# Performance work log

Hardware: AMD Instinct MI355X
Metric: run time of the kernel (lower is better)

Reference implementation:

```python
import jax, jax.numpy as jnp
import numpy as np

B, TXT, IMG, D, H = 1, 512, 2048, 1024, 16
HD = D // H
MLP = 4 * D
L = TXT + IMG

def _ln(x, s, b, eps=1e-6):
    mu = jnp.mean(x, -1, keepdims=True)
    var = jnp.var(x, -1, keepdims=True)
    return (x - mu) * jax.lax.rsqrt(var + eps) * s + b

def _rms(x, scale, eps=1e-6):
    return x * jax.lax.rsqrt(jnp.mean(x * x, -1, keepdims=True) + eps) * scale

def _rope(x, pe):
    # x: [B,H,L,HD] -> pairs [B,H,L,HD/2,1,2]; pe: [1,1,L,HD/2,2,2]
    xr = x.reshape(x.shape[0], x.shape[1], x.shape[2], -1, 1, 2)
    out = pe[..., 0] * xr[..., 0] + pe[..., 1] * xr[..., 1]
    return out.reshape(x.shape)

def _mod(vec, w, b):
    m = jax.nn.silu(vec) @ w + b  # [B, 6D]
    return jnp.split(m[:, None, :], 6, axis=-1)

def _stream_qkv(x, shift, scale, n1s, n1b, qkv_w, qkv_b, qs, ks):
    xm = (1 + scale) * _ln(x, n1s, n1b) + shift
    qkv = xm @ qkv_w + qkv_b  # [B,L,3D]
    b_, l_ = qkv.shape[0], qkv.shape[1]
    qkv = qkv.reshape(b_, l_, 3, H, HD).transpose(2, 0, 3, 1, 4)  # 'B L (K H D) -> K B H L D'
    q, k, v = qkv[0], qkv[1], qkv[2]
    return _rms(q, qs), _rms(k, ks), v

def _fwd(img, txt, vec, pe,
         img_mod_w, img_mod_b, img_norm1_s, img_norm1_b, img_qkv_w, img_qkv_b,
         img_qscale, img_kscale, img_proj_w, img_proj_b, img_norm2_s, img_norm2_b,
         img_mlp_w1, img_mlp_b1, img_mlp_w2, img_mlp_b2,
         txt_mod_w, txt_mod_b, txt_norm1_s, txt_norm1_b, txt_qkv_w, txt_qkv_b,
         txt_qscale, txt_kscale, txt_proj_w, txt_proj_b, txt_norm2_s, txt_norm2_b,
         txt_mlp_w1, txt_mlp_b1, txt_mlp_w2, txt_mlp_b2):
    i_sh1, i_sc1, i_g1, i_sh2, i_sc2, i_g2 = _mod(vec, img_mod_w, img_mod_b)
    t_sh1, t_sc1, t_g1, t_sh2, t_sc2, t_g2 = _mod(vec, txt_mod_w, txt_mod_b)
    iq, ik, iv = _stream_qkv(img, i_sh1, i_sc1, img_norm1_s, img_norm1_b, img_qkv_w, img_qkv_b, img_qscale, img_kscale)
    tq, tk, tv = _stream_qkv(txt, t_sh1, t_sc1, txt_norm1_s, txt_norm1_b, txt_qkv_w, txt_qkv_b, txt_qscale, txt_kscale)
    q = jnp.concatenate((tq, iq), axis=2)  # txt tokens first
    k = jnp.concatenate((tk, ik), axis=2)
    v = jnp.concatenate((tv, iv), axis=2)
    q = _rope(q, pe)
    k = _rope(k, pe)
    logits = jnp.einsum('bhqd,bhkd->bhqk', q, k) * (HD ** -0.5)
    attn = jnp.einsum('bhqk,bhkd->bhqd', jax.nn.softmax(logits, axis=-1), v)
    attn = attn.transpose(0, 2, 1, 3).reshape(q.shape[0], L, D)  # 'B H L D -> B L (H D)'
    t_attn, i_attn = attn[:, :TXT], attn[:, TXT:]
    img = img + i_g1 * (i_attn @ img_proj_w + img_proj_b)
    h = (1 + i_sc2) * _ln(img, img_norm2_s, img_norm2_b) + i_sh2
    img = img + i_g2 * (jax.nn.gelu(h @ img_mlp_w1 + img_mlp_b1) @ img_mlp_w2 + img_mlp_b2)
    txt = txt + t_g1 * (t_attn @ txt_proj_w + txt_proj_b)
    h = (1 + t_sc2) * _ln(txt, txt_norm2_s, txt_norm2_b) + t_sh2
    txt = txt + t_g2 * (jax.nn.gelu(h @ txt_mlp_w1 + txt_mlp_b1) @ txt_mlp_w2 + txt_mlp_b2)
    return img, txt

def setup_inputs():
    key = jax.random.key(0)
    keys = iter(jax.random.split(key, 80))
    def rn(shape, s=0.02):
        return jax.random.normal(next(keys), shape, jnp.float32) * s
    inp = {
        'img': jax.random.normal(next(keys), (B, IMG, D), jnp.float32),
        'txt': jax.random.normal(next(keys), (B, TXT, D), jnp.float32),
        'vec': jax.random.normal(next(keys), (B, D), jnp.float32),
        'pe': jax.random.normal(next(keys), (1, 1, L, HD // 2, 2, 2), jnp.float32),
    }
    for p in ('img', 'txt'):
        inp[p + '_mod_w'] = rn((D, 6 * D)); inp[p + '_mod_b'] = jnp.zeros((6 * D,), jnp.float32)
        inp[p + '_norm1_s'] = jnp.ones((D,), jnp.float32); inp[p + '_norm1_b'] = jnp.zeros((D,), jnp.float32)
        inp[p + '_qkv_w'] = rn((D, 3 * D)); inp[p + '_qkv_b'] = jnp.zeros((3 * D,), jnp.float32)
        inp[p + '_qscale'] = jnp.ones((HD,), jnp.float32); inp[p + '_kscale'] = jnp.ones((HD,), jnp.float32)
        inp[p + '_proj_w'] = rn((D, D)); inp[p + '_proj_b'] = jnp.zeros((D,), jnp.float32)
        inp[p + '_norm2_s'] = jnp.ones((D,), jnp.float32); inp[p + '_norm2_b'] = jnp.zeros((D,), jnp.float32)
        inp[p + '_mlp_w1'] = rn((D, MLP)); inp[p + '_mlp_b1'] = jnp.zeros((MLP,), jnp.float32)
        inp[p + '_mlp_w2'] = rn((MLP, D)); inp[p + '_mlp_b2'] = jnp.zeros((D,), jnp.float32)
    return inp

def reference(img, txt, vec, pe,
              img_mod_w, img_mod_b, img_norm1_s, img_norm1_b, img_qkv_w, img_qkv_b,
              img_qscale, img_kscale, img_proj_w, img_proj_b, img_norm2_s, img_norm2_b,
              img_mlp_w1, img_mlp_b1, img_mlp_w2, img_mlp_b2,
              txt_mod_w, txt_mod_b, txt_norm1_s, txt_norm1_b, txt_qkv_w, txt_qkv_b,
              txt_qscale, txt_kscale, txt_proj_w, txt_proj_b, txt_norm2_s, txt_norm2_b,
              txt_mlp_w1, txt_mlp_b1, txt_mlp_w2, txt_mlp_b2):
    return _fwd(img, txt, vec, pe,
                img_mod_w, img_mod_b, img_norm1_s, img_norm1_b, img_qkv_w, img_qkv_b,
                img_qscale, img_kscale, img_proj_w, img_proj_b, img_norm2_s, img_norm2_b,
                img_mlp_w1, img_mlp_b1, img_mlp_w2, img_mlp_b2,
                txt_mod_w, txt_mod_b, txt_norm1_s, txt_norm1_b, txt_qkv_w, txt_qkv_b,
                txt_qscale, txt_kscale, txt_proj_w, txt_proj_b, txt_norm2_s, txt_norm2_b,
                txt_mlp_w1, txt_mlp_b1, txt_mlp_w2, txt_mlp_b2)
```

## Files before the change

### kernel.cpp

```cpp
#include <hip/hip_runtime.h>
#include <cstdint>
#include <cstddef>

#define DD 1024
#define HD 64
#define NH 16
#define LTXT 512
#define LIMG 2048
#define LTOT 2560
#define DMLP 4096

typedef unsigned short u16;
typedef __attribute__((ext_vector_type(8))) __bf16 bf16x8;
typedef __attribute__((ext_vector_type(4))) float f32x4;

__device__ __forceinline__ u16 f2bf(float f) {
  union { float f; uint32_t u; } v; v.f = f;
  uint32_t r = v.u + 0x7FFFu + ((v.u >> 16) & 1u);
  return (u16)(r >> 16);
}
__device__ __forceinline__ float bf2f(u16 u) {
  union { uint32_t u; float f; } v; v.u = ((uint32_t)u) << 16;
  return v.f;
}
__device__ __forceinline__ uint32_t cvtpk(float lo, float hi) {
  uint32_t r;
  asm("v_cvt_pk_bf16_f32 %0, %1, %2" : "=v"(r) : "v"(lo), "v"(hi));
  return r;
}
__device__ __forceinline__ float geluf(float x) {
  const float u = fmaf(x * x, 0.044715f, 1.0f);
  const float e = __expf(x * u * -1.5957691216057308f);
  return x / (1.f + e);
}
__device__ __forceinline__ void gload16(const void* g, void* l) {
  __builtin_amdgcn_global_load_lds(
      (const __attribute__((address_space(1))) void*)g,
      (__attribute__((address_space(3))) void*)l, 16, 0, 0);
}
#define SWZ(row) (((((row) & 3) | ((((row) >> 3) & 1) << 2)) << 4))

__global__ __launch_bounds__(256) void wcast_all(
    const float* __restrict__ s0, const float* __restrict__ s1,
    const float* __restrict__ s2, const float* __restrict__ s3,
    const float* __restrict__ s4, const float* __restrict__ s5,
    const float* __restrict__ s6, const float* __restrict__ s7,
    u16* __restrict__ d0, u16* __restrict__ d1, u16* __restrict__ d2,
    u16* __restrict__ d3, u16* __restrict__ d4, u16* __restrict__ d5,
    u16* __restrict__ d6, u16* __restrict__ d7) {
  const int b = blockIdx.x;
  const float* W; u16* Wt; int K, N, lb;
  if (b < 768)       { W = s0; Wt = d0; K = 1024; N = 3072; lb = b; }
  else if (b < 1536) { W = s1; Wt = d1; K = 1024; N = 3072; lb = b - 768; }
  else if (b < 1792) { W = s2; Wt = d2; K = 1024; N = 1024; lb = b - 1536; }
  else if (b < 2048) { W = s3; Wt = d3; K = 1024; N = 1024; lb = b - 1792; }
  else if (b < 3072) { W = s4; Wt = d4; K = 1024; N = 4096; lb = b - 2048; }
  else if (b < 4096) { W = s5; Wt = d5; K = 1024; N = 4096; lb = b - 3072; }
  else if (b < 5120) { W = s6; Wt = d6; K = 4096; N = 1024; lb = b - 4096; }
  else               { W = s7; Wt = d7; K = 4096; N = 1024; lb = b - 5120; }
  const int ntn = N >> 6;
  const int n0 = (lb % ntn) * 64, k0 = (lb / ntn) * 64;
  __shared__ float T[64][65];
  const int tx = threadIdx.x & 15, ty = threadIdx.x >> 4;
#pragma unroll
  for (int i = 0; i < 4; ++i) {
    const int r = ty + i * 16;
    const float4 v = *(const float4*)&W[(size_t)(k0 + r) * N + n0 + tx * 4];
    T[r][tx * 4 + 0] = v.x;
    T[r][tx * 4 + 1] = v.y;
    T[r][tx * 4 + 2] = v.z;
    T[r][tx * 4 + 3] = v.w;
  }
  __syncthreads();
  const int rn = threadIdx.x >> 2;
  const int cs = (threadIdx.x & 3) * 16;
  u16 buf[16];
#pragma unroll
  for (int j = 0; j < 16; ++j) buf[j] = f2bf(T[cs + j][rn]);
  u16* dst = &Wt[(size_t)(n0 + rn) * K + k0 + cs];
  *(uint4*)dst = *(uint4*)&buf[0];
  *(uint4*)(dst + 8) = *(uint4*)&buf[8];
}

__global__ __launch_bounds__(256) void mod_gemv_part(
    const float* __restrict__ vec, const float* __restrict__ wi,
    const float* __restrict__ wt, float* __restrict__ part) {
  __shared__ float sv[128];
  const int s = blockIdx.y, kc = blockIdx.z;
  const float* W = s ? wt : wi;
  if (threadIdx.x < 128) {
    float x = vec[kc * 128 + threadIdx.x];
    sv[threadIdx.x] = x / (1.f + __expf(-x));
  }
  __syncthreads();
  const int j = blockIdx.x * 256 + threadIdx.x;
  float acc = 0.f;
#pragma unroll 4
  for (int i = 0; i < 128; ++i)
    acc += sv[i] * W[(size_t)(kc * 128 + i) * 6144 + j];
  part[((size_t)(kc * 2 + s)) * 6144 + j] = acc;
}
__global__ __launch_bounds__(256) void mod_reduce(
    const float* __restrict__ part, const float* __restrict__ bi,
    const float* __restrict__ bt, float* __restrict__ modout) {
  const int idx = blockIdx.x * 256 + threadIdx.x;
  const int s = idx / 6144, j = idx % 6144;
  float a = s ? bt[j] : bi[j];
#pragma unroll
  for (int kc = 0; kc < 8; ++kc) a += part[((size_t)(kc * 2 + s)) * 6144 + j];
  modout[(size_t)s * 6144 + j] = a;
}

__global__ __launch_bounds__(256) void ln_mod2(
    const float* __restrict__ Xtxt, const float* __restrict__ Ximg,
    u16* __restrict__ out, const float* __restrict__ tns,
    const float* __restrict__ tnb, const float* __restrict__ ins,
    const float* __restrict__ inb, const float* __restrict__ modv) {
  __shared__ float red[8];
  const int r = blockIdx.x, tid = threadIdx.x;
  const float* x; const float* ns; const float* nb; const float* mv;
  if (r < LTXT) { x = Xtxt + (size_t)r * DD; ns = tns; nb = tnb; mv = modv + 6144; }
  else { x = Ximg + (size_t)(r - LTXT) * DD; ns = ins; nb = inb; mv = modv; }
  const int c0 = tid * 4;
  const float4 xv = *(const float4*)&x[c0];
  float v[4] = {xv.x, xv.y, xv.z, xv.w};
  float s = 0.f, sq = 0.f;
#pragma unroll
  for (int i = 0; i < 4; ++i) { s += v[i]; sq += v[i] * v[i]; }
#pragma unroll
  for (int o = 32; o; o >>= 1) {
    s += __shfl_xor(s, o);
    sq += __shfl_xor(sq, o);
  }
  if ((tid & 63) == 0) {
    red[tid >> 6] = s;
    red[4 + (tid >> 6)] = sq;
  }
  __syncthreads();
  s = red[0] + red[1] + red[2] + red[3];
  sq = red[4] + red[5] + red[6] + red[7];
  const float mu = s * (1.f / DD);
  const float var = sq * (1.f / DD) - mu * mu;
  const float rstd = rsqrtf(var + 1e-6f);
  const float4 nsv = *(const float4*)&ns[c0];
  const float4 nbv = *(const float4*)&nb[c0];
  const float4 shv = *(const float4*)&mv[c0];
  const float4 scv = *(const float4*)&mv[1024 + c0];
  const float nsa[4] = {nsv.x, nsv.y, nsv.z, nsv.w};
  const float nba[4] = {nbv.x, nbv.y, nbv.z, nbv.w};
  const float sha[4] = {shv.x, shv.y, shv.z, shv.w};
  const float sca[4] = {scv.x, scv.y, scv.z, scv.w};
  ushort4 o4;
  u16 ob[4];
#pragma unroll
  for (int i = 0; i < 4; ++i) {
    const float ln = (v[i] - mu) * rstd * nsa[i] + nba[i];
    ob[i] = f2bf((1.f + sca[i]) * ln + sha[i]);
  }
  o4.x = ob[0]; o4.y = ob[1]; o4.z = ob[2]; o4.w = ob[3];
  *(ushort4*)&out[(size_t)r * DD + c0] = o4;
}

__global__ __launch_bounds__(256) void resid_ln2(
    const float* __restrict__ Xtxt, const float* __restrict__ Ximg,
    const u16* __restrict__ t, const float* __restrict__ modv,
    const float* __restrict__ tns, const float* __restrict__ tnb,
    const float* __restrict__ ins, const float* __restrict__ inb,
    float* __restrict__ otxt, float* __restrict__ oimg,
    u16* __restrict__ hout) {
  __shared__ float red[8];
  const int r = blockIdx.x, tid = threadIdx.x;
  const float* x; const float* ns; const float* nb; const float* mv; float* y;
  if (r < LTXT) {
    x = Xtxt + (size_t)r * DD; ns = tns; nb = tnb; mv = modv + 6144;
    y = otxt + (size_t)r * DD;
  } else {
    x = Ximg + (size_t)(r - LTXT) * DD; ns = ins; nb = inb; mv = modv;
    y = oimg + (size_t)(r - LTXT) * DD;
  }
  const int c0 = tid * 4;
  const float4 xv = *(const float4*)&x[c0];
  const ushort4 tb = *(const ushort4*)&t[(size_t)r * DD + c0];
  const float4 gv = *(const float4*)&mv[2048 + c0];
  float v[4];
  v[0] = xv.x + gv.x * bf2f(tb.x);
  v[1] = xv.y + gv.y * bf2f(tb.y);
  v[2] = xv.z + gv.z * bf2f(tb.z);
  v[3] = xv.w + gv.w * bf2f(tb.w);
  *(float4*)&y[c0] = *(float4*)v;
  float s = 0.f, sq = 0.f;
#pragma unroll
  for (int i = 0; i < 4; ++i) { s += v[i]; sq += v[i] * v[i]; }
#pragma unroll
  for (int o = 32; o; o >>= 1) {
    s += __shfl_xor(s, o);
    sq += __shfl_xor(sq, o);
  }
  if ((tid & 63) == 0) {
    red[tid >> 6] = s;
    red[4 + (tid >> 6)] = sq;
  }
  __syncthreads();
  s = red[0] + red[1] + red[2] + red[3];
  sq = red[4] + red[5] + red[6] + red[7];
  const float mu = s * (1.f / DD);
  const float var = sq * (1.f / DD) - mu * mu;
  const float rstd = rsqrtf(var + 1e-6f);
  const float4 nsv = *(const float4*)&ns[c0];
  const float4 nbv = *(const float4*)&nb[c0];
  const float4 shv = *(const float4*)&mv[3072 + c0];
  const float4 scv = *(const float4*)&mv[4096 + c0];
  const float nsa[4] = {nsv.x, nsv.y, nsv.z, nsv.w};
  const float nba[4] = {nbv.x, nbv.y, nbv.z, nbv.w};
  const float sha[4] = {shv.x, shv.y, shv.z, shv.w};
  const float sca[4] = {scv.x, scv.y, scv.z, scv.w};
  ushort4 o4;
  u16 ob[4];
#pragma unroll
  for (int i = 0; i < 4; ++i) {
    const float ln = (v[i] - mu) * rstd * nsa[i] + nba[i];
    ob[i] = f2bf((1.f + sca[i]) * ln + sha[i]);
  }
  o4.x = ob[0]; o4.y = ob[1]; o4.z = ob[2]; o4.w = ob[3];
  *(ushort4*)&hout[(size_t)r * DD + c0] = o4;
}

__global__ __launch_bounds__(512) void gemm_pipe(
    const u16* __restrict__ A, const u16* __restrict__ BtT,
    const u16* __restrict__ BtI, const float* __restrict__ biasT,
    const float* __restrict__ biasI, u16* __restrict__ C,
    float* __restrict__ Cpart, int K, int Kblk, int N, int gelu) {
  __shared__ __align__(16) u16 As[2][128 * 32];
  __shared__ __align__(16) u16 Bs[2][128 * 32];
  const int tid = threadIdx.x, lane = tid & 63, wave = tid >> 6;
  const int nwg = gridDim.x * gridDim.y;
  const int orig = blockIdx.x + blockIdx.y * gridDim.x;
  const int lb = (orig & 7) * (nwg >> 3) + (orig >> 3);
  const int bn = lb / 20, bm = lb % 20;
  const int kc = blockIdx.z;
  const u16* Bt = (bm < (LTXT / 128)) ? BtT : BtI;
  const int wm = wave >> 1, wn = wave & 1;
  const int lr = lane & 15, lk = lane >> 4;
  f32x4 acc[2][4] = {};
  const size_t a0 = (size_t)bm * 128;
  const size_t b0 = (size_t)bn * 128;
  const int kbase = kc * Kblk;
  const int NT = Kblk >> 5;
  const int srow = tid >> 2, soff = (tid & 3) * 8;

#define STAGE(t, buf)                                                         \
  {                                                                           \
    const int k0_ = kbase + (t) * 32;                                         \
    gload16(&A[(a0 + srow) * K + k0_ + soff], &As[buf][srow * 32 + soff]);    \
    gload16(&Bt[(b0 + srow) * K + k0_ + soff], &Bs[buf][srow * 32 + soff]);   \
  }

  STAGE(0, 0);
  STAGE(1, 1);
  for (int t = 0; t < NT; ++t) {
    if (t + 1 < NT) {
      asm volatile("s_waitcnt vmcnt(2)" ::: "memory");
    } else {
      asm volatile("s_waitcnt vmcnt(0)" ::: "memory");
    }
    __builtin_amdgcn_s_barrier();
    const int b = t & 1;
    bf16x8 af[2], bfv[4];
#pragma unroll
    for (int m = 0; m < 2; ++m)
      af[m] = *(const bf16x8*)&As[b][(wm * 32 + m * 16 + lr) * 32 + lk * 8];
#pragma unroll
    for (int n = 0; n < 4; ++n)
      bfv[n] = *(const bf16x8*)&Bs[b][(wn * 64 + n * 16 + lr) * 32 + lk * 8];
    asm volatile("s_waitcnt lgkmcnt(0)" ::: "memory");
    __builtin_amdgcn_sched_barrier(0);
    __builtin_amdgcn_s_barrier();
    if (t + 2 < NT) STAGE(t + 2, b);
    __builtin_amdgcn_sched_barrier(0);
    __builtin_amdgcn_s_setprio(1);
#pragma unroll
    for (int m = 0; m < 2; ++m)
#pragma unroll
      for (int n = 0; n < 4; ++n)
        acc[m][n] = __builtin_amdgcn_mfma_f32_16x16x32_bf16(af[m], bfv[n],
                                                            acc[m][n], 0, 0, 0);
    __builtin_amdgcn_s_setprio(0);
  }
#undef STAGE

  if (Cpart) {
    float* dst = Cpart + (size_t)kc * ((size_t)LTOT * N);
#pragma unroll
    for (int n = 0; n < 4; ++n) {
      const int col = bn * 128 + wn * 64 + n * 16 + lr;
#pragma unroll
      for (int m = 0; m < 2; ++m)
#pragma unroll
        for (int r = 0; r < 4; ++r) {
          const size_t row = a0 + wm * 32 + m * 16 + lk * 4 + r;
          dst[row * (size_t)N + col] = acc[m][n][r];
        }
    }
  } else {
    const float* bias = (bm < (LTXT / 128)) ? biasT : biasI;
#pragma unroll
    for (int n = 0; n < 4; ++n) {
      const int col = bn * 128 + wn * 64 + n * 16 + lr;
      const float bv = bias[col];
#pragma unroll
      for (int m = 0; m < 2; ++m)
#pragma unroll
        for (int r = 0; r < 4; ++r) {
          const size_t row = a0 + wm * 32 + m * 16 + lk * 4 + r;
          float v = acc[m][n][r] + bv;
          if (gelu) v = geluf(v);
          C[row * (size_t)N + col] = f2bf(v);
        }
    }
  }
}

__global__ __launch_bounds__(256) void gemm_reduce(
    const float* __restrict__ part, const float* __restrict__ bT,
    const float* __restrict__ bI, u16* __restrict__ C, int N, int kcnt) {
  const size_t idx = (size_t)(blockIdx.x * 256 + threadIdx.x) * 4;
  const int row = (int)(idx / N), col = (int)(idx % N);
  float4 a = *(const float4*)&part[idx];
  for (int kc = 1; kc < kcnt; ++kc) {
    const float4 b = *(const float4*)&part[(size_t)kc * LTOT * N + idx];
    a.x += b.x; a.y += b.y; a.z += b.z; a.w += b.w;
  }
  const float* bias = (row < LTXT) ? bT : bI;
  ushort4 o;
  o.x = f2bf(a.x + bias[col]);
  o.y = f2bf(a.y + bias[col + 1]);
  o.z = f2bf(a.z + bias[col + 2]);
  o.w = f2bf(a.w + bias[col + 3]);
  *(ushort4*)&C[idx] = o;
}

__global__ __launch_bounds__(256) void gemm_reduce_gate(
    const float* __restrict__ part, const float* __restrict__ bT,
    const float* __restrict__ bI, const float* __restrict__ modv,
    float* __restrict__ otxt, float* __restrict__ oimg, int kcnt) {
  const size_t idx = (size_t)(blockIdx.x * 256 + threadIdx.x) * 4;
  const int row = (int)(idx >> 10), col = (int)(idx & 1023);
  float4 a = *(const float4*)&part[idx];
  for (int kc = 1; kc < kcnt; ++kc) {
    const float4 b = *(const float4*)&part[(size_t)kc * LTOT * DD + idx];
    a.x += b.x; a.y += b.y; a.z += b.z; a.w += b.w;
  }
  const float* bias; const float* mv; float* o;
  if (row < LTXT) {
    bias = bT; mv = modv + 6144; o = otxt + (size_t)row * DD + col;
  } else {
    bias = bI; mv = modv; o = oimg + (size_t)(row - LTXT) * DD + col;
  }
  const float4 g = *(const float4*)&mv[5120 + col];
  const float4 cur = *(const float4*)o;
  float4 r;
  r.x = cur.x + g.x * (a.x + bias[col]);
  r.y = cur.y + g.y * (a.y + bias[col + 1]);
  r.z = cur.z + g.z * (a.z + bias[col + 2]);
  r.w = cur.w + g.w * (a.w + bias[col + 3]);
  *(float4*)o = r;
}

__global__ __launch_bounds__(256) void scat_rope(
    const u16* __restrict__ qkv, u16* __restrict__ q, u16* __restrict__ k,
    const float* __restrict__ pe, const float* __restrict__ iqs,
    const float* __restrict__ iks, const float* __restrict__ tqs,
    const float* __restrict__ tks) {
  const int gw = (blockIdx.x * 256 + threadIdx.x) >> 6;
  const int lane = threadIdx.x & 63;
  const int l = gw % LTOT, h = gw / LTOT;
  const size_t rb = (size_t)l * 3072 + h * 64 + lane;
  const float qv = bf2f(qkv[rb]);
  const float kv = bf2f(qkv[rb + 1024]);
  const float* qs = (l < LTXT) ? tqs : iqs;
  const float* ks = (l < LTXT) ? tks : iks;
  const float* peb = pe + (size_t)l * 128 + (lane >> 1) * 4 + (lane & 1) * 2;
  const size_t base = ((size_t)h * LTOT + l) * HD + lane;
  {
    float ss = qv * qv;
#pragma unroll
    for (int o = 32; o; o >>= 1) ss += __shfl_xor(ss, o);
    float xn = qv * rsqrtf(ss * (1.f / HD) + 1e-6f) * qs[lane];
    float part = __shfl_xor(xn, 1);
    float x0 = (lane & 1) ? part : xn;
    float x1 = (lane & 1) ? xn : part;
    q[base] = f2bf(peb[0] * x0 + peb[1] * x1);
  }
  {
    float ss = kv * kv;
#pragma unroll
    for (int o = 32; o; o >>= 1) ss += __shfl_xor(ss, o);
    float xn = kv * rsqrtf(ss * (1.f / HD) + 1e-6f) * ks[lane];
    float part = __shfl_xor(xn, 1);
    float x0 = (lane & 1) ? part : xn;
    float x1 = (lane & 1) ? xn : part;
    k[base] = f2bf(peb[0] * x0 + peb[1] * x1);
  }
}

__global__ __launch_bounds__(256) void vt_build(const u16* __restrict__ qkv,
                                                u16* __restrict__ vt) {
  __shared__ u16 T[64][72];
  const int b = blockIdx.x;
  const int h = b & 15, lt = b >> 4;
  const int tid = threadIdx.x;
  const int r = tid >> 3, c8 = (tid & 7) * 8;
  const size_t srcbase = (size_t)(lt * 64) * 3072 + 2048 + h * 64;
  *(uint4*)&T[r][c8] = *(const uint4*)&qkv[srcbase + (size_t)r * 3072 + c8];
  *(uint4*)&T[r + 32][c8] =
      *(const uint4*)&qkv[srcbase + (size_t)(r + 32) * 3072 + c8];
  __syncthreads();
  const int d = tid >> 2, lc = (tid & 3) * 16;
  u16 buf[16];
#pragma unroll
  for (int j = 0; j < 16; ++j) buf[j] = T[lc + j][d];
  u16* dst = &vt[((size_t)h * 64 + d) * LTOT + lt * 64 + lc];
  *(uint4*)dst = *(uint4*)&buf[0];
  *(uint4*)(dst + 8) = *(uint4*)&buf[8];
}

template <int SPLIT>
__global__ __launch_bounds__(512) void attn_mfma(
    const u16* __restrict__ Q, const u16* __restrict__ Kg,
    const u16* __restrict__ VT, u16* __restrict__ out,
    float* __restrict__ part) {
  constexpr int LOG = (SPLIT == 4) ? 2 : ((SPLIT == 2) ? 1 : 0);
  __shared__ __align__(16) u16 Ks[2][64 * 64];
  __shared__ __align__(16) u16 Vs[2][64 * 64];
  const int tid = threadIdx.x, lane = tid & 63, w = tid >> 6;
  const int lr = lane & 15, lk = lane >> 4;
  const int blk = blockIdx.x;
  const int h = ((blk & 7) << 1) | ((blk >> 3) & 1);
  const int half = (blk >> 4) & (SPLIT - 1);
  const int q0 = (blk >> (4 + LOG)) * 128;
  const size_t hb = (size_t)h * LTOT;
  char* KsB0 = (char*)&Ks[0][0];
  char* VsB0 = (char*)&Vs[0][0];

  const int q = q0 + w * 16 + lr;
  const bf16x8 qa0 = *(const bf16x8*)&Q[(hb + q) * HD + lk * 8];
  const bf16x8 qa1 = *(const bf16x8*)&Q[(hb + q) * HD + 32 + lk * 8];

  const int srow = tid >> 3;
  const int soff = tid & 7;
  const int NT = (LTOT / SPLIT) / 64;
  const int kstart = half * (LTOT / SPLIT);

  float m_run = -1e30f, l_run = 0.f;
  f32x4 acc[4] = {};
  uint4 kst, vst;

  kst = *(const uint4*)&Kg[(hb + kstart + srow) * HD + soff * 8];
  vst = *(const uint4*)&VT[((size_t)h * HD + srow) * LTOT + kstart + soff * 8];
  *(uint4*)(KsB0 + ((srow * 128 + soff * 16) ^ SWZ(srow))) = kst;
  *(uint4*)(VsB0 + ((srow * 128 + soff * 16) ^ SWZ(srow))) = vst;
  __syncthreads();

  const float scale = 0.125f;
  for (int t = 0; t < NT; ++t) {
    char* KsC = KsB0 + (t & 1) * 8192;
    char* VsC = VsB0 + (t & 1) * 8192;
    if (t + 1 < NT) {
      const int k0n = kstart + (t + 1) * 64;
      kst = *(const uint4*)&Kg[(hb + k0n + srow) * HD + soff * 8];
      vst = *(const uint4*)&VT[((size_t)h * HD + srow) * LTOT + k0n + soff * 8];
    }
    f32x4 s[4];
    __builtin_amdgcn_s_setprio(1);
#pragma unroll
    for (int g = 0; g < 4; ++g) {
      const int kr = (lr >> 2) * 8 + (g & 1) * 4 + (lr & 3) + (g >> 1) * 32;
      const int sw = SWZ(kr);
      const bf16x8 ka0 = *(const bf16x8*)(KsC + ((kr * 128 + lk * 16) ^ sw));
      const bf16x8 ka1 = *(const bf16x8*)(KsC + ((kr * 128 + 64 + lk * 16) ^ sw));
      f32x4 z = {0.f, 0.f, 0.f, 0.f};
      z = __builtin_amdgcn_mfma_f32_16x16x32_bf16(ka0, qa0, z, 0, 0, 0);
      z = __builtin_amdgcn_mfma_f32_16x16x32_bf16(ka1, qa1, z, 0, 0, 0);
      s[g] = z;
    }
    __builtin_amdgcn_s_setprio(0);
    float gm[4];
#pragma unroll
    for (int g = 0; g < 4; ++g)
      gm[g] = fmaxf(fmaxf(s[g][0], s[g][1]), fmaxf(s[g][2], s[g][3]));
    float tmax = fmaxf(fmaxf(gm[0], gm[1]), fmaxf(gm[2], gm[3]));
    tmax = fmaxf(tmax, __shfl_xor(tmax, 16));
    tmax = fmaxf(tmax, __shfl_xor(tmax, 32));
    tmax *= scale;
    if (!__all(tmax <= m_run + 8.f)) {
      const float mnew = fmaxf(m_run, tmax);
      const float alpha = __expf(m_run - mnew);
      l_run *= alpha;
#pragma unroll
      for (int dt = 0; dt < 4; ++dt) {
        acc[dt][0] *= alpha;
        acc[dt][1] *= alpha;
        acc[dt][2] *= alpha;
        acc[dt][3] *= alpha;
      }
      m_run = mnew;
    }
    float p[4][4];
    float psum = 0.f;
#pragma unroll
    for (int g = 0; g < 4; ++g)
#pragma unroll
      for (int r = 0; r < 4; ++r) {
        p[g][r] = __expf(s[g][r] * scale - m_run);
        psum += p[g][r];
      }
    psum += __shfl_xor(psum, 16);
    psum += __shfl_xor(psum, 32);
    l_run += psum;
    union { uint32_t u[4]; bf16x8 v; } pb0, pb1;
    pb0.u[0] = cvtpk(p[0][0], p[0][1]);
    pb0.u[1] = cvtpk(p[0][2], p[0][3]);
    pb0.u[2] = cvtpk(p[1][0], p[1][1]);
    pb0.u[3] = cvtpk(p[1][2], p[1][3]);
    pb1.u[0] = cvtpk(p[2][0], p[2][1]);
    pb1.u[1] = cvtpk(p[2][2], p[2][3]);
    pb1.u[2] = cvtpk(p[3][0], p[3][1]);
    pb1.u[3] = cvtpk(p[3][2], p[3][3]);
    __builtin_amdgcn_s_setprio(1);
#pragma unroll
    for (int dt = 0; dt < 4; ++dt) {
      const int vr = dt * 16 + lr;
      const int sw = SWZ(vr);
      const bf16x8 va0 = *(const bf16x8*)(VsC + ((vr * 128 + lk * 16) ^ sw));
      const bf16x8 va1 = *(const bf16x8*)(VsC + ((vr * 128 + 64 + lk * 16) ^ sw));
      acc[dt] = __builtin_amdgcn_mfma_f32_16x16x32_bf16(va0, pb0.v, acc[dt], 0, 0, 0);
      acc[dt] = __builtin_amdgcn_mfma_f32_16x16x32_bf16(va1, pb1.v, acc[dt], 0, 0, 0);
    }
    __builtin_amdgcn_s_setprio(0);
    if (t + 1 < NT) {
      char* KsN = KsB0 + ((t + 1) & 1) * 8192;
      char* VsN = VsB0 + ((t + 1) & 1) * 8192;
      *(uint4*)(KsN + ((srow * 128 + soff * 16) ^ SWZ(srow))) = kst;
      *(uint4*)(VsN + ((srow * 128 + soff * 16) ^ SWZ(srow))) = vst;
      __syncthreads();
    }
  }
  if (SPLIT > 1) {
    float* pr = part + (((size_t)(half * LTOT) + q) * 16 + h) * 68;
#pragma unroll
    for (int dt = 0; dt < 4; ++dt)
      *(f32x4*)&pr[dt * 16 + lk * 4] = acc[dt];
    if (lk == 0) {
      pr[64] = m_run;
      pr[65] = l_run;
    }
  } else {
    __syncthreads();
    const float inv = 1.f / l_run;
    char* ob = KsB0 + w * 2048;
    const int esw = (lr & 7) << 4;
#pragma unroll
    for (int dt = 0; dt < 4; ++dt) {
      const uint32_t a = cvtpk(acc[dt][0] * inv, acc[dt][1] * inv);
      const uint32_t b2 = cvtpk(acc[dt][2] * inv, acc[dt][3] * inv);
      const int ad = lr * 128 + dt * 32 + lk * 8;
      *(uint32_t*)(ob + (ad ^ esw)) = a;
      *(uint32_t*)(ob + ((ad + 4) ^ esw)) = b2;
    }
    __syncthreads();
    const int row = lane >> 2, ch = lane & 3;
    const int rsw = (row & 7) << 4;
    const uint4 o0 = *(const uint4*)(ob + ((row * 128 + ch * 32) ^ rsw));
    const uint4 o1 = *(const uint4*)(ob + ((row * 128 + ch * 32 + 16) ^ rsw));
    u16* orow = &out[(size_t)(q0 + w * 16 + row) * DD + h * HD + ch * 16];
    *(uint4*)orow = o0;
    *(uint4*)(orow + 8) = o1;
  }
}

template <int SPLIT>
__global__ __launch_bounds__(256) void attn_merge(const float* __restrict__ part,
                                                  u16* __restrict__ out) {
  const int idx = blockIdx.x * 256 + threadIdx.x;
  const int d4 = idx & 15, h = (idx >> 4) & 15, q = idx >> 8;
  size_t base[SPLIT];
  float ms[SPLIT], ls[SPLIT];
  float m = -1e30f;
#pragma unroll
  for (int s = 0; s < SPLIT; ++s) {
    base[s] = (((size_t)(s * LTOT) + q) * 16 + h) * 68;
    ms[s] = part[base[s] + 64];
    ls[s] = part[base[s] + 65];
    m = fmaxf(m, ms[s]);
  }
  float denom = 0.f;
  float a[SPLIT];
#pragma unroll
  for (int s = 0; s < SPLIT; ++s) {
    a[s] = __expf(ms[s] - m);
    denom += ls[s] * a[s];
  }
  const float inv = 1.f / denom;
  float r[4] = {0.f, 0.f, 0.f, 0.f};
#pragma unroll
  for (int s = 0; s < SPLIT; ++s) {
    const float4 x = *(const float4*)&part[base[s] + d4 * 4];
    const float sc = a[s] * inv;
    r[0] += x.x * sc; r[1] += x.y * sc; r[2] += x.z * sc; r[3] += x.w * sc;
  }
  uint2 o;
  o.x = cvtpk(r[0], r[1]);
  o.y = cvtpk(r[2], r[3]);
  *(uint2*)&out[(size_t)q * DD + h * HD + d4 * 4] = o;
}

__global__ __launch_bounds__(256) void resid_gate(
    const float* __restrict__ xin, const u16* __restrict__ t,
    const float* __restrict__ g, float* __restrict__ out, int n4) {
  const int idx = blockIdx.x * 256 + threadIdx.x;
  if (idx >= n4) return;
  const int col = (idx * 4) & (DD - 1);
  const float4 a = ((const float4*)xin)[idx];
  const ushort4 tb = ((const ushort4*)t)[idx];
  const float4 gg = *(const float4*)&g[col];
  float4 r;
  r.x = a.x + gg.x * bf2f(tb.x);
  r.y = a.y + gg.y * bf2f(tb.y);
  r.z = a.z + gg.z * bf2f(tb.z);
  r.w = a.w + gg.w * bf2f(tb.w);
  ((float4*)out)[idx] = r;
}

extern "C" void kernel_launch(void* const* d_in, const int* in_sizes, int n_in,
                              void* d_out, int out_size, void* d_ws,
                              size_t ws_size, hipStream_t stream) {
  const float* img = (const float*)d_in[0];
  const float* txt = (const float*)d_in[1];
  const float* vec = (const float*)d_in[2];
  const float* pe = (const float*)d_in[3];
  const float* i_mod_w = (const float*)d_in[4];
  const float* i_mod_b = (const float*)d_in[5];
  const float* i_n1s = (const float*)d_in[6];
  const float* i_n1b = (const float*)d_in[7];
  const float* i_qkv_w = (const float*)d_in[8];
  const float* i_qkv_b = (const float*)d_in[9];
  const float* i_qs = (const float*)d_in[10];
  const float* i_ks = (const float*)d_in[11];
  const float* i_proj_w = (const float*)d_in[12];
  const float* i_proj_b = (const float*)d_in[13];
  const float* i_n2s = (const float*)d_in[14];
  const float* i_n2b = (const float*)d_in[15];
  const float* i_w1 = (const float*)d_in[16];
  const float* i_b1 = (const float*)d_in[17];
  const float* i_w2 = (const float*)d_in[18];
  const float* i_b2 = (const float*)d_in[19];
  const float* t_mod_w = (const float*)d_in[20];
  const float* t_mod_b = (const float*)d_in[21];
  const float* t_n1s = (const float*)d_in[22];
  const float* t_n1b = (const float*)d_in[23];
  const float* t_qkv_w = (const float*)d_in[24];
  const float* t_qkv_b = (const float*)d_in[25];
  const float* t_qs = (const float*)d_in[26];
  const float* t_ks = (const float*)d_in[27];
  const float* t_proj_w = (const float*)d_in[28];
  const float* t_proj_b = (const float*)d_in[29];
  const float* t_n2s = (const float*)d_in[30];
  const float* t_n2b = (const float*)d_in[31];
  const float* t_w1 = (const float*)d_in[32];
  const float* t_b1 = (const float*)d_in[33];
  const float* t_w2 = (const float*)d_in[34];
  const float* t_b2 = (const float*)d_in[35];

  const size_t LD = (size_t)LTOT * DD;
  uint8_t* p = (uint8_t*)d_ws;
  float* modb = (float*)p;           p += 64 * 1024;
  float* part = (float*)p;           p += 512 * 1024;
  u16* tqkvT = (u16*)p;              p += (size_t)3072 * 1024 * 2;
  u16* iqkvT = (u16*)p;              p += (size_t)3072 * 1024 * 2;
  u16* tprojT = (u16*)p;             p += (size_t)1024 * 1024 * 2;
  u16* iprojT = (u16*)p;             p += (size_t)1024 * 1024 * 2;
  u16* tw1T = (u16*)p;               p += (size_t)4096 * 1024 * 2;
  u16* iw1T = (u16*)p;               p += (size_t)4096 * 1024 * 2;
  u16* tw2T = (u16*)p;               p += (size_t)1024 * 4096 * 2;
  u16* iw2T = (u16*)p;               p += (size_t)1024 * 4096 * 2;
  u16* actA = (u16*)p;               p += LD * 2;
  u16* actB = (u16*)p;               p += (size_t)LTOT * DMLP * 2;
  u16* actC = (u16*)p;               p += LD * 2 * 3;
  float* gpart = (float*)p;
  const size_t used = (size_t)(p - (uint8_t*)d_ws);
  const size_t avail = ws_size > used ? ws_size - used : 0;
  const size_t attn_need2 = (size_t)2 * LTOT * 16 * 68 * sizeof(float);
  const size_t attn_need4 = 2 * attn_need2;
  const int attn_split = avail >= attn_need4 ? 4 : (avail >= attn_need2 ? 2 : 1);
  const int kc_proj = avail >= 2 * LD * sizeof(float) ? 2 : 1;
  const int kc_mlp2 = avail >= 4 * LD * sizeof(float)
                          ? 4
                          : (avail >= 2 * LD * sizeof(float) ? 2 : 1);
  float* out_img = (float*)d_out;
  float* out_txt = out_img + (size_t)LIMG * DD;

  wcast_all<<<6144, 256, 0, stream>>>(t_qkv_w, i_qkv_w, t_proj_w, i_proj_w,
                                      t_w1, i_w1, t_w2, i_w2, tqkvT, iqkvT,
                                      tprojT, iprojT, tw1T, iw1T, tw2T, iw2T);
  mod_gemv_part<<<dim3(24, 2, 8), 256, 0, stream>>>(vec, i_mod_w, t_mod_w, part);
  mod_reduce<<<48, 256, 0, stream>>>(part, i_mod_b, t_mod_b, modb);
  ln_mod2<<<LTOT, 256, 0, stream>>>(txt, img, actA, t_n1s, t_n1b, i_n1s, i_n1b,
                                    modb);
  gemm_pipe<<<dim3(24, 20, 1), 512, 0, stream>>>(actA, tqkvT, iqkvT, t_qkv_b,
                                                 i_qkv_b, actB, nullptr, 1024,
                                                 1024, 3072, 0);
  scat_rope<<<10240, 256, 0, stream>>>(actB, actC, actC + LD, pe, i_qs, i_ks,
                                       t_qs, t_ks);
  vt_build<<<640, 256, 0, stream>>>(actB, actC + 2 * LD);
  if (attn_split == 4) {
    attn_mfma<4><<<1280, 512, 0, stream>>>(actC, actC + LD, actC + 2 * LD,
                                           actA, gpart);
    attn_merge<4><<<2560, 256, 0, stream>>>(gpart, actA);
  } else if (attn_split == 2) {
    attn_mfma<2><<<640, 512, 0, stream>>>(actC, actC + LD, actC + 2 * LD,
                                          actA, gpart);
    attn_merge<2><<<2560, 256, 0, stream>>>(gpart, actA);
  } else {
    attn_mfma<1><<<320, 512, 0, stream>>>(actC, actC + LD, actC + 2 * LD, actA,
                                          nullptr);
  }
  if (kc_proj > 1) {
    gemm_pipe<<<dim3(8, 20, kc_proj), 512, 0, stream>>>(
        actA, tprojT, iprojT, nullptr, nullptr, nullptr, gpart, 1024,
        1024 / kc_proj, 1024, 0);
    gemm_reduce<<<2560, 256, 0, stream>>>(gpart, t_proj_b, i_proj_b, actC,
                                          1024, kc_proj);
  } else {
    gemm_pipe<<<dim3(8, 20, 1), 512, 0, stream>>>(actA, tprojT, iprojT,
                                                  t_proj_b, i_proj_b, actC,
                                                  nullptr, 1024, 1024, 1024, 0);
  }
  resid_ln2<<<LTOT, 256, 0, stream>>>(txt, img, actC, modb, t_n2s, t_n2b,
                                      i_n2s, i_n2b, out_txt, out_img,
                                      actC + LD);
  gemm_pipe<<<dim3(32, 20, 1), 512, 0, stream>>>(actC + LD, tw1T, iw1T, t_b1,
                                                 i_b1, actB, nullptr, 1024,
                                                 1024, 4096, 1);
  if (kc_mlp2 > 1) {
    gemm_pipe<<<dim3(8, 20, kc_mlp2), 512, 0, stream>>>(
        actB, tw2T, iw2T, nullptr, nullptr, nullptr, gpart, 4096,
        4096 / kc_mlp2, 1024, 0);
    gemm_reduce_gate<<<2560, 256, 0, stream>>>(gpart, t_b2, i_b2, modb,
                                               out_txt, out_img, kc_mlp2);
  } else {
    gemm_pipe<<<dim3(8, 20, 1), 512, 0, stream>>>(actB, tw2T, iw2T, t_b2, i_b2,
                                                  actC + 2 * LD, nullptr, 4096,
                                                  4096, 1024, 0);
    resid_gate<<<2048, 256, 0, stream>>>(out_img,
                                         actC + 2 * LD + (size_t)LTXT * DD,
                                         modb + 5120, out_img, LIMG * DD / 4);
    resid_gate<<<512, 256, 0, stream>>>(out_txt, actC + 2 * LD,
                                        modb + 6144 + 5120, out_txt,
                                        LTXT * DD / 4);
  }
}
```

Measured before the change: 264.2 us.

## Fold softmax scale and log2e into Q, use exp2, store bf16 attention partials

Measured after the change: 258.8 us. 1.02x faster.

```diff
diff --git a/kernel.cpp b/kernel.cpp
--- a/kernel.cpp
+++ b/kernel.cpp
@@ -27,6 +27,9 @@
   uint32_t r;
   asm("v_cvt_pk_bf16_f32 %0, %1, %2" : "=v"(r) : "v"(lo), "v"(hi));
   return r;
+}
+__device__ __forceinline__ float fexp2(float x) {
+  return __builtin_amdgcn_exp2f(x);
 }
 __device__ __forceinline__ float geluf(float x) {
   const float u = fmaf(x * x, 0.044715f, 1.0f);
@@ -389,7 +392,7 @@
     float part = __shfl_xor(xn, 1);
     float x0 = (lane & 1) ? part : xn;
     float x1 = (lane & 1) ? xn : part;
-    q[base] = f2bf(peb[0] * x0 + peb[1] * x1);
+    q[base] = f2bf((peb[0] * x0 + peb[1] * x1) * 0.1803368801111f);
   }
   {
     float ss = kv * kv;
@@ -428,7 +431,7 @@
 __global__ __launch_bounds__(512) void attn_mfma(
     const u16* __restrict__ Q, const u16* __restrict__ Kg,
     const u16* __restrict__ VT, u16* __restrict__ out,
-    float* __restrict__ part) {
+    u16* __restrict__ part) {
   constexpr int LOG = (SPLIT == 4) ? 2 : ((SPLIT == 2) ? 1 : 0);
   __shared__ __align__(16) u16 Ks[2][64 * 64];
   __shared__ __align__(16) u16 Vs[2][64 * 64];
@@ -461,7 +464,6 @@
   *(uint4*)(VsB0 + ((srow * 128 + soff * 16) ^ SWZ(srow))) = vst;
   __syncthreads();
 
-  const float scale = 0.125f;
   for (int t = 0; t < NT; ++t) {
     char* KsC = KsB0 + (t & 1) * 8192;
     char* VsC = VsB0 + (t & 1) * 8192;
@@ -491,10 +493,9 @@
     float tmax = fmaxf(fmaxf(gm[0], gm[1]), fmaxf(gm[2], gm[3]));
     tmax = fmaxf(tmax, __shfl_xor(tmax, 16));
     tmax = fmaxf(tmax, __shfl_xor(tmax, 32));
-    tmax *= scale;
-    if (!__all(tmax <= m_run + 8.f)) {
+    if (!__all(tmax <= m_run + 11.5415603f)) {
       const float mnew = fmaxf(m_run, tmax);
-      const float alpha = __expf(m_run - mnew);
+      const float alpha = fexp2(m_run - mnew);
       l_run *= alpha;
 #pragma unroll
       for (int dt = 0; dt < 4; ++dt) {
@@ -511,7 +512,7 @@
     for (int g = 0; g < 4; ++g)
 #pragma unroll
       for (int r = 0; r < 4; ++r) {
-        p[g][r] = __expf(s[g][r] * scale - m_run);
+        p[g][r] = fexp2(s[g][r] - m_run);
         psum += p[g][r];
       }
     psum += __shfl_xor(psum, 16);
@@ -546,13 +547,17 @@
     }
   }
   if (SPLIT > 1) {
-    float* pr = part + (((size_t)(half * LTOT) + q) * 16 + h) * 68;
-#pragma unroll
-    for (int dt = 0; dt < 4; ++dt)
-      *(f32x4*)&pr[dt * 16 + lk * 4] = acc[dt];
+    u16* pr = part + (((size_t)(half * LTOT) + q) * 16 + h) * 80;
+#pragma unroll
+    for (int dt = 0; dt < 4; ++dt) {
+      uint2 o;
+      o.x = cvtpk(acc[dt][0], acc[dt][1]);
+      o.y = cvtpk(acc[dt][2], acc[dt][3]);
+      *(uint2*)&pr[dt * 16 + lk * 4] = o;
+    }
     if (lk == 0) {
-      pr[64] = m_run;
-      pr[65] = l_run;
+      *(float*)&pr[64] = m_run;
+      *(float*)&pr[66] = l_run;
     }
   } else {
     __syncthreads();
@@ -579,34 +584,38 @@
 }
 
 template <int SPLIT>
-__global__ __launch_bounds__(256) void attn_merge(const float* __restrict__ part,
+__global__ __launch_bounds__(256) void attn_merge(const u16* __restrict__ part,
                                                   u16* __restrict__ out) {
   const int idx = blockIdx.x * 256 + threadIdx.x;
   const int d4 = idx & 15, h = (idx >> 4) & 15, q = idx >> 8;
-  size_t base[SPLIT];
+  const u16* bp[SPLIT];
   float ms[SPLIT], ls[SPLIT];
   float m = -1e30f;
 #pragma unroll
   for (int s = 0; s < SPLIT; ++s) {
-    base[s] = (((size_t)(s * LTOT) + q) * 16 + h) * 68;
-    ms[s] = part[base[s] + 64];
-    ls[s] = part[base[s] + 65];
+    bp[s] = part + (((size_t)(s * LTOT) + q) * 16 + h) * 80;
+    ms[s] = *(const float*)&bp[s][64];
+    ls[s] = *(const float*)&bp[s][66];
     m = fmaxf(m, ms[s]);
   }
   float denom = 0.f;
   float a[SPLIT];
 #pragma unroll
   for (int s = 0; s < SPLIT; ++s) {
-    a[s] = __expf(ms[s] - m);
+    a[s] = fexp2(ms[s] - m);
     denom += ls[s] * a[s];
   }
   const float inv = 1.f / denom;
   float r[4] = {0.f, 0.f, 0.f, 0.f};
 #pragma unroll
   for (int s = 0; s < SPLIT; ++s) {
-    const float4 x = *(const float4*)&part[base[s] + d4 * 4];
+    const uint2 xr = *(const uint2*)&bp[s][d4 * 4];
+    const u16* xp = (const u16*)&xr;
     const float sc = a[s] * inv;
-    r[0] += x.x * sc; r[1] += x.y * sc; r[2] += x.z * sc; r[3] += x.w * sc;
+    r[0] += bf2f(xp[0]) * sc;
+    r[1] += bf2f(xp[1]) * sc;
+    r[2] += bf2f(xp[2]) * sc;
+    r[3] += bf2f(xp[3]) * sc;
   }
   uint2 o;
   o.x = cvtpk(r[0], r[1]);
@@ -689,7 +698,7 @@
   float* gpart = (float*)p;
   const size_t used = (size_t)(p - (uint8_t*)d_ws);
   const size_t avail = ws_size > used ? ws_size - used : 0;
-  const size_t attn_need2 = (size_t)2 * LTOT * 16 * 68 * sizeof(float);
+  const size_t attn_need2 = (size_t)2 * LTOT * 16 * 80 * sizeof(u16);
   const size_t attn_need4 = 2 * attn_need2;
   const int attn_split = avail >= attn_need4 ? 4 : (avail >= attn_need2 ? 2 : 1);
   const int kc_proj = avail >= 2 * LD * sizeof(float) ? 2 : 1;
@@ -714,12 +723,12 @@
   vt_build<<<640, 256, 0, stream>>>(actB, actC + 2 * LD);
   if (attn_split == 4) {
     attn_mfma<4><<<1280, 512, 0, stream>>>(actC, actC + LD, actC + 2 * LD,
-                                           actA, gpart);
-    attn_merge<4><<<2560, 256, 0, stream>>>(gpart, actA);
+                                           actA, (u16*)gpart);
+    attn_merge<4><<<2560, 256, 0, stream>>>((const u16*)gpart, actA);
   } else if (attn_split == 2) {
     attn_mfma<2><<<640, 512, 0, stream>>>(actC, actC + LD, actC + 2 * LD,
-                                          actA, gpart);
-    attn_merge<2><<<2560, 256, 0, stream>>>(gpart, actA);
+                                          actA, (u16*)gpart);
+    attn_merge<2><<<2560, 256, 0, stream>>>((const u16*)gpart, actA);
   } else {
     attn_mfma<1><<<320, 512, 0, stream>>>(actC, actC + LD, actC + 2 * LD, actA,
                                           nullptr);
```
